# Optimization experiments

Hardware: AMD Instinct MI355X
Metric: run time of the kernel (lower is better)

## Reference

```python
import jax, jax.numpy as jnp
import numpy as np


def setup_inputs() -> dict:
    key = jax.random.key(0)
    k1, k2 = jax.random.split(key)
    x = jax.random.normal(k1, (16, 64, 512, 512), dtype=jnp.float32)
    # Conv2d(2, 1, kernel_size=7, bias=False): weight [out=1, in=2, 7, 7]
    fan_in = 2 * 7 * 7
    bound = 1.0 / np.sqrt(fan_in)
    w = jax.random.uniform(k2, (1, 2, 7, 7), dtype=jnp.float32, minval=-bound, maxval=bound)
    return {"x": x, "w": w}


def reference(x, w):
    # channel-wise max and mean, keepdim -> [B,1,H,W] each
    mx = jnp.max(x, axis=1, keepdims=True)
    avg = jnp.mean(x, axis=1, keepdims=True)
    a = jnp.concatenate([mx, avg], axis=1)  # [B,2,H,W]
    # 7x7 conv, padding=3, NCHW/OIHW
    y = jax.lax.conv_general_dilated(
        a, w,
        window_strides=(1, 1),
        padding=((3, 3), (3, 3)),
        dimension_numbers=("NCHW", "OIHW", "NCHW"),
    )
    return jax.nn.sigmoid(y)  # [B,1,H,W]
```

## Files before the change

kernel.cpp:

```cpp
#include <hip/hip_runtime.h>
#include <math.h>

#define W 512
#define H 512
#define HW (512 * 512)
#define CC 64
#define BB 16

__global__ __launch_bounds__(256) void reduce_kernel(const float* __restrict__ x,
                                                     float* __restrict__ planes) {
    const int perB = HW / 4;
    int t = blockIdx.x * 256 + threadIdx.x;
    int b = t >> 16;
    int p = t & 65535;

    const float4* xb = reinterpret_cast<const float4*>(x) + (size_t)b * CC * perB + p;

    float4 v = xb[0];
    float4 mx = v;
    float4 sm = v;
    #pragma unroll 8
    for (int c = 1; c < CC; ++c) {
        float4 u = xb[(size_t)c * perB];
        mx.x = fmaxf(mx.x, u.x);
        mx.y = fmaxf(mx.y, u.y);
        mx.z = fmaxf(mx.z, u.z);
        mx.w = fmaxf(mx.w, u.w);
        sm.x += u.x;
        sm.y += u.y;
        sm.z += u.z;
        sm.w += u.w;
    }
    const float inv = 1.0f / (float)CC;
    float4 av = make_float4(sm.x * inv, sm.y * inv, sm.z * inv, sm.w * inv);

    float4* outb = reinterpret_cast<float4*>(planes) + (size_t)b * 2 * perB;
    outb[p] = mx;
    outb[perB + p] = av;
}

__global__ __launch_bounds__(256) void conv_kernel(const float* __restrict__ planes,
                                                   const float* __restrict__ wgt,
                                                   float* __restrict__ out) {
    __shared__ float2 sm[38][40];

    const int b   = blockIdx.z;
    const int th0 = blockIdx.y * 32;
    const int tw0 = blockIdx.x * 32;
    const int tid = threadIdx.y * 32 + threadIdx.x;

    const float* pb = planes + (size_t)b * 2 * HW;

    for (int i = tid; i < 38 * 38; i += 256) {
        int r = i / 38, c = i - r * 38;
        int h = th0 + r - 3;
        int w = tw0 + c - 3;
        float vmax = 0.0f, vavg = 0.0f;
        if (h >= 0 && h < H && w >= 0 && w < W) {
            vmax = pb[h * W + w];
            vavg = pb[HW + h * W + w];
        }
        sm[r][c] = make_float2(vmax, vavg);
    }

    float wm[49], wa[49];
    #pragma unroll
    for (int i = 0; i < 49; ++i) {
        wm[i] = wgt[i];
        wa[i] = wgt[49 + i];
    }

    __syncthreads();

    const int tx = threadIdx.x;
    const int ty = threadIdx.y;

    float acc0 = 0.f, acc1 = 0.f, acc2 = 0.f, acc3 = 0.f;
    #pragma unroll
    for (int r = 0; r < 10; ++r) {
        #pragma unroll
        for (int kw = 0; kw < 7; ++kw) {
            float2 v = sm[4 * ty + r][tx + kw];
            #pragma unroll
            for (int k = 0; k < 4; ++k) {
                int kh = r - k;
                if (kh >= 0 && kh < 7) {
                    float a = (k == 0) ? acc0 : (k == 1) ? acc1 : (k == 2) ? acc2 : acc3;
                    a = fmaf(v.x, wm[kh * 7 + kw], a);
                    a = fmaf(v.y, wa[kh * 7 + kw], a);
                    if (k == 0) acc0 = a; else if (k == 1) acc1 = a; else if (k == 2) acc2 = a; else acc3 = a;
                }
            }
        }
    }

    float* ob = out + (size_t)b * HW + (size_t)tw0 + tx;
    {
        int h = th0 + 4 * ty;
        ob[(h + 0) * W] = 1.0f / (1.0f + __expf(-acc0));
        ob[(h + 1) * W] = 1.0f / (1.0f + __expf(-acc1));
        ob[(h + 2) * W] = 1.0f / (1.0f + __expf(-acc2));
        ob[(h + 3) * W] = 1.0f / (1.0f + __expf(-acc3));
    }
}

extern "C" void kernel_launch(void* const* d_in, const int* in_sizes, int n_in,
                              void* d_out, int out_size, void* d_ws, size_t ws_size,
                              hipStream_t stream) {
    const float* x   = (const float*)d_in[0];
    const float* wgt = (const float*)d_in[1];
    float* out = (float*)d_out;
    float* planes = (float*)d_ws;

    reduce_kernel<<<dim3(4096), dim3(256), 0, stream>>>(x, planes);

    conv_kernel<<<dim3(16, 16, 16), dim3(32, 8), 0, stream>>>(planes, wgt, out);
}
```

Before: 234.2 us.

## Store reduced planes as interleaved fp16 and use nontemporal wider loads

```diff
diff --git a/kernel.cpp b/kernel.cpp
--- a/kernel.cpp
+++ b/kernel.cpp
@@ -1,4 +1,5 @@
 #include <hip/hip_runtime.h>
+#include <hip/hip_fp16.h>
 #include <math.h>
 
 #define W 512
@@ -7,39 +8,53 @@
 #define CC 64
 #define BB 16
 
+typedef float f32x4 __attribute__((ext_vector_type(4)));
+
 __global__ __launch_bounds__(256) void reduce_kernel(const float* __restrict__ x,
-                                                     float* __restrict__ planes) {
+                                                     __half2* __restrict__ planes) {
     const int perB = HW / 4;
     int t = blockIdx.x * 256 + threadIdx.x;
-    int b = t >> 16;
-    int p = t & 65535;
+    int b = t >> 15;
+    int p = (t & 32767) * 2;
 
-    const float4* xb = reinterpret_cast<const float4*>(x) + (size_t)b * CC * perB + p;
+    const f32x4* xb = reinterpret_cast<const f32x4*>(x) + (size_t)b * CC * perB + p;
 
-    float4 v = xb[0];
-    float4 mx = v;
-    float4 sm = v;
+    f32x4 mx0 = __builtin_nontemporal_load(xb);
+    f32x4 mx1 = __builtin_nontemporal_load(xb + 1);
+    f32x4 sm0 = mx0, sm1 = mx1;
+
     #pragma unroll 8
     for (int c = 1; c < CC; ++c) {
-        float4 u = xb[(size_t)c * perB];
-        mx.x = fmaxf(mx.x, u.x);
-        mx.y = fmaxf(mx.y, u.y);
-        mx.z = fmaxf(mx.z, u.z);
-        mx.w = fmaxf(mx.w, u.w);
-        sm.x += u.x;
-        sm.y += u.y;
-        sm.z += u.z;
-        sm.w += u.w;
+        const f32x4* q = xb + (size_t)c * perB;
+        f32x4 a = __builtin_nontemporal_load(q);
+        f32x4 bq = __builtin_nontemporal_load(q + 1);
+        mx0.x = fmaxf(mx0.x, a.x);  sm0.x += a.x;
+        mx0.y = fmaxf(mx0.y, a.y);  sm0.y += a.y;
+        mx0.z = fmaxf(mx0.z, a.z);  sm0.z += a.z;
+        mx0.w = fmaxf(mx0.w, a.w);  sm0.w += a.w;
+        mx1.x = fmaxf(mx1.x, bq.x); sm1.x += bq.x;
+        mx1.y = fmaxf(mx1.y, bq.y); sm1.y += bq.y;
+        mx1.z = fmaxf(mx1.z, bq.z); sm1.z += bq.z;
+        mx1.w = fmaxf(mx1.w, bq.w); sm1.w += bq.w;
     }
+
     const float inv = 1.0f / (float)CC;
-    float4 av = make_float4(sm.x * inv, sm.y * inv, sm.z * inv, sm.w * inv);
+    __half2 h[8];
+    h[0] = __floats2half2_rn(mx0.x, sm0.x * inv);
+    h[1] = __floats2half2_rn(mx0.y, sm0.y * inv);
+    h[2] = __floats2half2_rn(mx0.z, sm0.z * inv);
+    h[3] = __floats2half2_rn(mx0.w, sm0.w * inv);
+    h[4] = __floats2half2_rn(mx1.x, sm1.x * inv);
+    h[5] = __floats2half2_rn(mx1.y, sm1.y * inv);
+    h[6] = __floats2half2_rn(mx1.z, sm1.z * inv);
+    h[7] = __floats2half2_rn(mx1.w, sm1.w * inv);
 
-    float4* outb = reinterpret_cast<float4*>(planes) + (size_t)b * 2 * perB;
-    outb[p] = mx;
-    outb[perB + p] = av;
+    uint4* dst = reinterpret_cast<uint4*>(planes + (size_t)b * HW + p * 4);
+    dst[0] = *reinterpret_cast<uint4*>(&h[0]);
+    dst[1] = *reinterpret_cast<uint4*>(&h[4]);
 }
 
-__global__ __launch_bounds__(256) void conv_kernel(const float* __restrict__ planes,
+__global__ __launch_bounds__(256) void conv_kernel(const __half2* __restrict__ planes,
                                                    const float* __restrict__ wgt,
                                                    float* __restrict__ out) {
     __shared__ float2 sm[38][40];
@@ -49,18 +64,17 @@
     const int tw0 = blockIdx.x * 32;
     const int tid = threadIdx.y * 32 + threadIdx.x;
 
-    const float* pb = planes + (size_t)b * 2 * HW;
+    const __half2* pb = planes + (size_t)b * HW;
 
     for (int i = tid; i < 38 * 38; i += 256) {
         int r = i / 38, c = i - r * 38;
         int h = th0 + r - 3;
         int w = tw0 + c - 3;
-        float vmax = 0.0f, vavg = 0.0f;
+        float2 v = make_float2(0.0f, 0.0f);
         if (h >= 0 && h < H && w >= 0 && w < W) {
-            vmax = pb[h * W + w];
-            vavg = pb[HW + h * W + w];
+            v = __half22float2(pb[h * W + w]);
         }
-        sm[r][c] = make_float2(vmax, vavg);
+        sm[r][c] = v;
     }
 
     float wm[49], wa[49];
@@ -110,9 +124,9 @@
     const float* x   = (const float*)d_in[0];
     const float* wgt = (const float*)d_in[1];
     float* out = (float*)d_out;
-    float* planes = (float*)d_ws;
+    __half2* planes = (__half2*)d_ws;
 
-    reduce_kernel<<<dim3(4096), dim3(256), 0, stream>>>(x, planes);
+    reduce_kernel<<<dim3(2048), dim3(256), 0, stream>>>(x, planes);
 
     conv_kernel<<<dim3(16, 16, 16), dim3(32, 8), 0, stream>>>(planes, wgt, out);
 }
```

New measurement: 232.2 us. Within noise of the previous version (-0.9%).
